# Kernel optimization log

Hardware: AMD Instinct MI355X
Metric: run time of the kernel (lower is better)

Reference implementation:

```python
import jax, jax.numpy as jnp
import numpy as np

B, I, O, DEG = 16384, 1024, 1024, 8

def setup_inputs() -> dict:
    key = jax.random.key(0)
    kx, kc = jax.random.split(key)
    x = jax.random.normal(kx, (B, I), dtype=jnp.float32)
    std = 1.0 / (I * (DEG + 1))
    cheby_coeffs = jax.random.normal(kc, (I, O, DEG + 1), dtype=jnp.float32) * std
    return {"x": x, "cheby_coeffs": cheby_coeffs}


def reference(x, cheby_coeffs):
    # Chebyshev basis: T_d(tanh(x)) = cos(d * acos(tanh(x)))
    deg = cheby_coeffs.shape[-1]
    arange = jnp.arange(deg, dtype=x.dtype)  # (D+1,)
    theta = jnp.arccos(jnp.tanh(x))          # (B, I)
    basis = jnp.cos(theta[:, :, None] * arange)  # (B, I, D+1)
    y = jnp.einsum('bid,iod->bo', basis, cheby_coeffs)
    return y
```

## Files before the change

kernel.cpp:

```cpp
#include <hip/hip_runtime.h>
#include <hip/hip_bf16.h>


#define WSCALE 4096.0f
#define INV_WSCALE (1.0f/4096.0f)

typedef _Float16 f16;
typedef __fp16   hf2  __attribute__((ext_vector_type(2)));
typedef _Float16 f16x8 __attribute__((ext_vector_type(8)));
typedef float    f32x4 __attribute__((ext_vector_type(4)));
typedef float    f32x16 __attribute__((ext_vector_type(16)));

union F16x8u { hf2 h2[4]; f16x8 v8; };

__global__ __launch_bounds__(256) void wt_transform(const float* __restrict__ cc,
                                                    f16* __restrict__ wt) {
  int t    = blockIdx.x * 256 + threadIdx.x;
  int j4   = t & 127;
  int grp  = t >> 7;
  int ncol = grp & 7;
  int rest = grp >> 3;
  int ic   = rest & 31;
  int d    = rest >> 5;
  int u    = j4 >> 5;
  int h    = (j4 >> 4) & 1;
  int r    = j4 & 15;
  int rk   = (r >> 1) & 3;
  size_t base = (size_t)(d * 32 + ic) * 32768 + (size_t)ncol * 4096 + (size_t)j4 * 32;
#pragma unroll
  for (int v = 0; v < 4; ++v) {
    int tt = v ^ rk;
    int q  = tt & 1, kl = tt >> 1;
    int o  = ncol * 128 + u * 32 + q * 16 + r;
    int ib = ic * 32 + h * 16 + kl * 8;
    f16x8 val;
#pragma unroll
    for (int e = 0; e < 8; ++e)
      val[e] = (f16)(cc[((size_t)(ib + e) * 1024 + o) * 9 + d] * WSCALE);
    *(f16x8*)(wt + base + v * 8) = val;
  }
}

__global__ __launch_bounds__(256) void t2_transform(const float* __restrict__ x,
                                                    f16* __restrict__ t2) {
  size_t gid = (size_t)blockIdx.x * 256 + threadIdx.x;
  const float* p = x + gid * 8;
  f32x4 a = *(const f32x4*)p;
  f32x4 b = *(const f32x4*)(p + 4);
  float tf[8];
#pragma unroll
  for (int e = 0; e < 8; ++e) {
    float xx = (e < 4) ? a[e] : b[e - 4];
    tf[e] = 1.f - 2.f * __builtin_amdgcn_rcpf(__expf(2.f * xx) + 1.f);
  }
  F16x8u u;
#pragma unroll
  for (int q = 0; q < 4; ++q)
    u.h2[q] = __builtin_amdgcn_cvt_pkrtz(tf[2 * q], tf[2 * q + 1]);
  f16x8 v = u.v8 + u.v8;
  *(f16x8*)(t2 + gid * 8) = v;
}

__global__ __launch_bounds__(256, 3) void cheby_gemm(const f16* __restrict__ t2g,
                                                     const f16* __restrict__ wt,
                                                     float* __restrict__ out) {
  __shared__ f16 bbuf[5][4096];

  const int tid  = threadIdx.x;
  const int wid  = tid >> 6;
  const int lane = tid & 63;
  const int lr   = lane & 31;
  const int lh   = lane >> 5;
  const int wm   = wid >> 1;
  const int wn   = wid & 1;
  const int mrow = blockIdx.x >> 3;
  const int ncol = blockIdx.x & 7;
  const int m0   = mrow * 128 + wm * 64;
  const int n0   = ncol * 128 + wn * 64;
  const int rbase = wn * 2048 + ((lane & 15) * 4 + ((lane >> 4) ^ ((lane >> 1) & 3))) * 8;

  auto stage = [&](int cn, int dn, int slot) {
    const f16* src = wt + (size_t)(dn * 32 + cn) * 32768 + (size_t)ncol * 4096;
    __builtin_amdgcn_global_load_lds(
        (const __attribute__((address_space(1))) unsigned*)(src + tid * 8),
        (__attribute__((address_space(3))) unsigned*)(&bbuf[slot][wid * 512]),
        16, 0, 0);
    __builtin_amdgcn_global_load_lds(
        (const __attribute__((address_space(1))) unsigned*)(src + 2048 + tid * 8),
        (__attribute__((address_space(3))) unsigned*)(&bbuf[slot][wid * 512 + 2048]),
        16, 0, 0);
  };

  f32x16 acc[2][2];
#pragma unroll
  for (int a = 0; a < 2; ++a)
#pragma unroll
    for (int b = 0; b < 2; ++b)
#pragma unroll
      for (int j = 0; j < 16; ++j) acc[a][b][j] = 0.f;

  const f16x8 ones  = {(f16)1,(f16)1,(f16)1,(f16)1,(f16)1,(f16)1,(f16)1,(f16)1};
  const f16x8 half8 = {(f16)0.5f,(f16)0.5f,(f16)0.5f,(f16)0.5f,
                       (f16)0.5f,(f16)0.5f,(f16)0.5f,(f16)0.5f};
  f16x8 t2v[2][2], t2n[2][2];

  auto loadx = [&](int cn) {
#pragma unroll
    for (int mb = 0; mb < 2; ++mb)
#pragma unroll
      for (int h = 0; h < 2; ++h)
        t2n[mb][h] = *(const f16x8*)(t2g + (size_t)(m0 + mb * 32 + lr) * 1024
                                         + cn * 32 + h * 16 + lh * 8);
  };

#define REC(NEW, S1, S2)                                                       \
  _Pragma("unroll") for (int mb = 0; mb < 2; ++mb)                             \
    _Pragma("unroll") for (int h = 0; h < 2; ++h)                              \
      NEW[mb][h] = __builtin_elementwise_fma(t2v[mb][h], S1[mb][h], -S2[mb][h]);

#define LOADB(BD, SLOT)                                                        \
  {                                                                            \
    const f16* bb = &bbuf[0][0] + (SLOT) * 4096 + rbase;                       \
    BD[0][0] = *(const f16x8*)&bb[0];    BD[0][1] = *(const f16x8*)&bb[512];   \
    BD[1][0] = *(const f16x8*)&bb[1024]; BD[1][1] = *(const f16x8*)&bb[1536];  \
  }

#define MFMA8(AF, BD)                                                          \
  {                                                                            \
    _Pragma("unroll") for (int nb = 0; nb < 2; ++nb)                           \
      _Pragma("unroll") for (int mb = 0; mb < 2; ++mb) {                       \
        acc[mb][nb] = __builtin_amdgcn_mfma_f32_32x32x16_f16(AF[mb][0], BD[nb][0], \
                                                             acc[mb][nb], 0, 0, 0); \
        acc[mb][nb] = __builtin_amdgcn_mfma_f32_32x32x16_f16(AF[mb][1], BD[nb][1], \
                                                             acc[mb][nb], 0, 0, 0); \
      }                                                                        \
  }

#define VMB(N)                                                                 \
  asm volatile("s_waitcnt vmcnt(" #N ")" ::: "memory");                        \
  __builtin_amdgcn_s_barrier();

  loadx(0);
  int p0 = 0, p1 = 1, p2 = 2, p3 = 3, p4 = 4;
  stage(0, 0, p0); stage(0, 1, p1); stage(0, 2, p2); stage(0, 3, p3);

  f16x8 onesA[2][2];
#pragma unroll
  for (int mb = 0; mb < 2; ++mb)
#pragma unroll
    for (int h = 0; h < 2; ++h) onesA[mb][h] = ones;

  f16x8 bfA[2][2], bfB[2][2];
  f16x8 A1[2][2], A2[2][2], A3[2][2], A4[2][2], A5[2][2], A6[2][2], A7[2][2], A8[2][2];

  for (int c = 0; c < 31; ++c) {
    VMB(4)
    LOADB(bfA, p0)
#pragma unroll
    for (int mb = 0; mb < 2; ++mb)
#pragma unroll
      for (int h = 0; h < 2; ++h) {
        t2v[mb][h] = t2n[mb][h];
        A1[mb][h]  = t2v[mb][h] * half8;
      }
    stage(c, 4, p4);
    loadx(c + 1);
    LOADB(bfB, p1)
    MFMA8(onesA, bfA)

    VMB(8) stage(c, 5, p0); LOADB(bfA, p2) REC(A2, A1, onesA) MFMA8(A1, bfB)
    VMB(8) stage(c, 6, p1); LOADB(bfB, p3) REC(A3, A2, A1)    MFMA8(A2, bfA)
    VMB(8) stage(c, 7, p2); LOADB(bfA, p4) REC(A4, A3, A2)    MFMA8(A3, bfB)
    VMB(4) stage(c, 8, p3); LOADB(bfB, p0) REC(A5, A4, A3)    MFMA8(A4, bfA)
    VMB(4) stage(c + 1, 0, p4); LOADB(bfA, p1) REC(A6, A5, A4) MFMA8(A5, bfB)
    VMB(4) stage(c + 1, 1, p0); LOADB(bfB, p2) REC(A7, A6, A5) MFMA8(A6, bfA)
    VMB(4) stage(c + 1, 2, p1); LOADB(bfA, p3) REC(A8, A7, A6) MFMA8(A7, bfB)
    stage(c + 1, 3, p2);
    MFMA8(A8, bfA)

    int tmp = p4; p4 = p3; p3 = p2; p2 = p1; p1 = p0; p0 = tmp;
  }

  {
    VMB(4)
    LOADB(bfA, p0)
#pragma unroll
    for (int mb = 0; mb < 2; ++mb)
#pragma unroll
      for (int h = 0; h < 2; ++h) {
        t2v[mb][h] = t2n[mb][h];
        A1[mb][h]  = t2v[mb][h] * half8;
      }
    stage(31, 4, p4);
    LOADB(bfB, p1)
    MFMA8(onesA, bfA)

    VMB(4) stage(31, 5, p0); LOADB(bfA, p2) REC(A2, A1, onesA) MFMA8(A1, bfB)
    VMB(4) stage(31, 6, p1); LOADB(bfB, p3) REC(A3, A2, A1)    MFMA8(A2, bfA)
    VMB(4) stage(31, 7, p2); LOADB(bfA, p4) REC(A4, A3, A2)    MFMA8(A3, bfB)
    VMB(4) stage(31, 8, p3); LOADB(bfB, p0) REC(A5, A4, A3)    MFMA8(A4, bfA)
    VMB(4) LOADB(bfA, p1) REC(A6, A5, A4) MFMA8(A5, bfB)
    VMB(2) LOADB(bfB, p2) REC(A7, A6, A5) MFMA8(A6, bfA)
    VMB(0) LOADB(bfA, p3) REC(A8, A7, A6) MFMA8(A7, bfB)
    MFMA8(A8, bfA)
  }
#undef REC
#undef LOADB
#undef MFMA8
#undef VMB

#pragma unroll
  for (int mb = 0; mb < 2; ++mb)
#pragma unroll
    for (int nb = 0; nb < 2; ++nb)
#pragma unroll
      for (int j = 0; j < 16; ++j) {
        int row = m0 + mb * 32 + 4 * lh + (j & 3) + 8 * (j >> 2);
        int col = n0 + nb * 32 + lr;
        out[(size_t)row * 1024 + col] = acc[mb][nb][j] * INV_WSCALE;
      }
}

__global__ __launch_bounds__(512, 2) void cheby_gemm_fb(const float* __restrict__ x,
                                                        const f16* __restrict__ wt,
                                                        float* __restrict__ out) {
  __shared__ f16 bbuf[18][4096];
  const int tid  = threadIdx.x;
  const int wid  = tid >> 6;
  const int lane = tid & 63;
  const int lr   = lane & 31;
  const int lh   = lane >> 5;
  const int wm   = wid >> 1;
  const int wn   = wid & 1;
  const int mrow = blockIdx.x >> 3;
  const int ncol = blockIdx.x & 7;
  const int m0   = mrow * 256 + wm * 64;
  const int n0   = ncol * 128 + wn * 64;
  const int rbase = wn * 2048 + ((lane & 15) * 4 + ((lane >> 4) ^ ((lane >> 1) & 3))) * 8;

  auto stage = [&](int cn, int dn, int buf) {
    const f16* src = wt + (size_t)(dn * 32 + cn) * 32768 + (size_t)ncol * 4096;
    __builtin_amdgcn_global_load_lds(
        (const __attribute__((address_space(1))) unsigned*)(src + tid * 8),
        (__attribute__((address_space(3))) unsigned*)(&bbuf[buf][wid * 512]),
        16, 0, 0);
  };
  auto stage9 = [&](int cn, int b0) {
#pragma unroll
    for (int d = 0; d < 9; ++d) stage(cn, d, b0 + d);
  };

  f32x16 acc[2][2];
#pragma unroll
  for (int a = 0; a < 2; ++a)
#pragma unroll
    for (int b = 0; b < 2; ++b)
#pragma unroll
      for (int j = 0; j < 16; ++j) acc[a][b][j] = 0.f;

  const f16x8 ones  = {(f16)1,(f16)1,(f16)1,(f16)1,(f16)1,(f16)1,(f16)1,(f16)1};
  const f16x8 half8 = {(f16)0.5f,(f16)0.5f,(f16)0.5f,(f16)0.5f,
                       (f16)0.5f,(f16)0.5f,(f16)0.5f,(f16)0.5f};
  f16x8 t2v[2][2], t2n[2][2];
  f32x4 xf[2][2][2];

  auto loadx = [&](int cn) {
#pragma unroll
    for (int mb = 0; mb < 2; ++mb)
#pragma unroll
      for (int h = 0; h < 2; ++h) {
        const float* p = x + (size_t)(m0 + mb * 32 + lr) * 1024 + cn * 32 + h * 16 + lh * 8;
        xf[mb][h][0] = *(const f32x4*)p;
        xf[mb][h][1] = *(const f32x4*)(p + 4);
      }
  };
  auto dotanh = [&]() {
#pragma unroll
    for (int mb = 0; mb < 2; ++mb)
#pragma unroll
      for (int h = 0; h < 2; ++h) {
        float tf[8];
#pragma unroll
        for (int e = 0; e < 8; ++e) {
          float xx = (e < 4) ? xf[mb][h][0][e] : xf[mb][h][1][e - 4];
          tf[e] = 1.f - 2.f * __builtin_amdgcn_rcpf(__expf(2.f * xx) + 1.f);
        }
        F16x8u u;
#pragma unroll
        for (int q = 0; q < 4; ++q)
          u.h2[q] = __builtin_amdgcn_cvt_pkrtz(tf[2 * q], tf[2 * q + 1]);
        t2n[mb][h] = u.v8 + u.v8;
      }
  };

#define REC(NEW, S1, S2)                                                       \
  _Pragma("unroll") for (int mb = 0; mb < 2; ++mb)                             \
    _Pragma("unroll") for (int h = 0; h < 2; ++h)                              \
      NEW[mb][h] = __builtin_elementwise_fma(t2v[mb][h], S1[mb][h], -S2[mb][h]);
#define CLUSTER(AF, DIDX)                                                      \
  {                                                                            \
    const f16* bb = &bbuf[0][0] + sbase + (DIDX) * 4096 + rbase;               \
    f16x8 bf[2][2];                                                            \
    _Pragma("unroll") for (int nb = 0; nb < 2; ++nb)                           \
      _Pragma("unroll") for (int h = 0; h < 2; ++h)                            \
        bf[nb][h] = *(const f16x8*)&bb[nb * 1024 + h * 512];                   \
    _Pragma("unroll") for (int nb = 0; nb < 2; ++nb)                           \
      _Pragma("unroll") for (int mb = 0; mb < 2; ++mb) {                       \
        acc[mb][nb] = __builtin_amdgcn_mfma_f32_32x32x16_f16(AF[mb][0], bf[nb][0], \
                                                             acc[mb][nb], 0, 0, 0); \
        acc[mb][nb] = __builtin_amdgcn_mfma_f32_32x32x16_f16(AF[mb][1], bf[nb][1], \
                                                             acc[mb][nb], 0, 0, 0); \
      }                                                                        \
  }

  stage9(0, 0);
  loadx(0);
  dotanh();

  f16x8 onesA[2][2];
#pragma unroll
  for (int mb = 0; mb < 2; ++mb)
#pragma unroll
    for (int h = 0; h < 2; ++h) onesA[mb][h] = ones;

  for (int c = 0; c < 32; ++c) {
    const bool lastc = (c == 31);
    const int  sbase = (c & 1) * 36864;
    const int  nbase = (1 - (c & 1)) * 9;

    asm volatile("s_waitcnt vmcnt(8)" ::: "memory");
    __builtin_amdgcn_s_barrier();

    f16x8 A1[2][2], A2[2][2], A3[2][2], A4[2][2], A5[2][2], A6[2][2], A7[2][2], A8[2][2];
#pragma unroll
    for (int mb = 0; mb < 2; ++mb)
#pragma unroll
      for (int h = 0; h < 2; ++h) {
        t2v[mb][h] = t2n[mb][h];
        A1[mb][h]  = t2v[mb][h] * half8;
      }
    if (!lastc) { stage9(c + 1, nbase); loadx(c + 1); }

    CLUSTER(onesA, 0)
    CLUSTER(A1, 1)
    REC(A2, A1, onesA)  CLUSTER(A2, 2)
    REC(A3, A2, A1)     CLUSTER(A3, 3)
    REC(A4, A3, A2)     CLUSTER(A4, 4)
    REC(A5, A4, A3)     CLUSTER(A5, 5)
    REC(A6, A5, A4)     CLUSTER(A6, 6)
    REC(A7, A6, A5)     CLUSTER(A7, 7)
    REC(A8, A7, A6)     CLUSTER(A8, 8)
    if (!lastc) dotanh();
  }
#undef REC
#undef CLUSTER

#pragma unroll
  for (int mb = 0; mb < 2; ++mb)
#pragma unroll
    for (int nb = 0; nb < 2; ++nb)
#pragma unroll
      for (int j = 0; j < 16; ++j) {
        int row = m0 + mb * 32 + 4 * lh + (j & 3) + 8 * (j >> 2);
        int col = n0 + nb * 32 + lr;
        out[(size_t)row * 1024 + col] = acc[mb][nb][j] * INV_WSCALE;
      }
}

extern "C" void kernel_launch(void* const* d_in, const int* in_sizes, int n_in,
                              void* d_out, int out_size, void* d_ws, size_t ws_size,
                              hipStream_t stream) {
  const float* x  = (const float*)d_in[0];
  const float* cc = (const float*)d_in[1];
  f16*   wt  = (f16*)d_ws;
  f16*   t2  = (f16*)((char*)d_ws + 18874368);
  float* out = (float*)d_out;

  hipLaunchKernelGGL(wt_transform, dim3(1152), dim3(256), 0, stream, cc, wt);
  if (ws_size >= 52428800) {
    hipLaunchKernelGGL(t2_transform, dim3(8192), dim3(256), 0, stream, x, t2);
    hipLaunchKernelGGL(cheby_gemm, dim3(1024), dim3(256), 0, stream, t2, wt, out);
  } else {
    hipLaunchKernelGGL(cheby_gemm_fb, dim3(512), dim3(512), 0, stream, x, wt, out);
  }
}
```

Before: 331.7 us.

## Coalesce weight transform via LDS and deepen GEMM LDS pipeline to six slots

```diff
diff --git a/kernel.cpp b/kernel.cpp
--- a/kernel.cpp
+++ b/kernel.cpp
@@ -7,37 +7,70 @@
 
 typedef _Float16 f16;
 typedef __fp16   hf2  __attribute__((ext_vector_type(2)));
+typedef _Float16 f16x2v __attribute__((ext_vector_type(2)));
 typedef _Float16 f16x8 __attribute__((ext_vector_type(8)));
 typedef float    f32x4 __attribute__((ext_vector_type(4)));
+typedef float    f32x4u __attribute__((ext_vector_type(4), aligned(4)));
+typedef float    f32x2u __attribute__((ext_vector_type(2), aligned(4)));
 typedef float    f32x16 __attribute__((ext_vector_type(16)));
 
 union F16x8u { hf2 h2[4]; f16x8 v8; };
 
 __global__ __launch_bounds__(256) void wt_transform(const float* __restrict__ cc,
                                                     f16* __restrict__ wt) {
-  int t    = blockIdx.x * 256 + threadIdx.x;
-  int j4   = t & 127;
-  int grp  = t >> 7;
-  int ncol = grp & 7;
-  int rest = grp >> 3;
-  int ic   = rest & 31;
-  int d    = rest >> 5;
-  int u    = j4 >> 5;
-  int h    = (j4 >> 4) & 1;
-  int r    = j4 & 15;
-  int rk   = (r >> 1) & 3;
-  size_t base = (size_t)(d * 32 + ic) * 32768 + (size_t)ncol * 4096 + (size_t)j4 * 32;
-#pragma unroll
-  for (int v = 0; v < 4; ++v) {
-    int tt = v ^ rk;
-    int q  = tt & 1, kl = tt >> 1;
-    int o  = ncol * 128 + u * 32 + q * 16 + r;
-    int ib = ic * 32 + h * 16 + kl * 8;
-    f16x8 val;
-#pragma unroll
-    for (int e = 0; e < 8; ++e)
-      val[e] = (f16)(cc[((size_t)(ib + e) * 1024 + o) * 9 + d] * WSCALE);
-    *(f16x8*)(wt + base + v * 8) = val;
+  __shared__ f16 s16[9216];
+  const int bid  = blockIdx.x;
+  const int u    = bid & 3;
+  const int ncol = (bid >> 2) & 7;
+  const int ic   = bid >> 5;
+  const int t    = threadIdx.x;
+  const int i2   = t >> 4;
+  const int o2   = t & 15;
+  const int i0   = i2 * 2, o0 = o2 * 2;
+  const int h    = i0 >> 4;
+  const int kl   = (i0 >> 3) & 1;
+  const int e    = i0 & 7;
+
+  float va[2][18];
+#pragma unroll
+  for (int ii = 0; ii < 2; ++ii) {
+    const float* g = cc + ((size_t)(ic * 32 + i0 + ii) * 1024
+                           + (ncol * 128 + u * 32 + o0)) * 9;
+    f32x4u a = *(const f32x4u*)(g);
+    f32x4u b = *(const f32x4u*)(g + 4);
+    f32x4u c4 = *(const f32x4u*)(g + 8);
+    f32x4u d4 = *(const f32x4u*)(g + 12);
+    f32x2u e2 = *(const f32x2u*)(g + 16);
+#pragma unroll
+    for (int j = 0; j < 4; ++j) { va[ii][j] = a[j]; va[ii][4 + j] = b[j];
+                                  va[ii][8 + j] = c4[j]; va[ii][12 + j] = d4[j]; }
+    va[ii][16] = e2[0]; va[ii][17] = e2[1];
+  }
+
+#pragma unroll
+  for (int oo = 0; oo < 2; ++oo) {
+    const int ol = o0 + oo;
+    const int r  = ol & 15, q = ol >> 4;
+    const int rk = (r >> 1) & 3;
+    const int vsl = (kl * 2 + q) ^ rk;
+    const int jj = h * 16 + r;
+#pragma unroll
+    for (int d = 0; d < 9; ++d) {
+      f16x2v pv = { (f16)(va[0][oo * 9 + d] * WSCALE),
+                    (f16)(va[1][oo * 9 + d] * WSCALE) };
+      *(f16x2v*)(&s16[(d * 128 + jj * 4 + vsl) * 8 + e]) = pv;
+    }
+  }
+  __syncthreads();
+
+#pragma unroll
+  for (int w = 0; w < 5; ++w) {
+    int cidx = t + 256 * w;
+    if (cidx < 1152) {
+      f16x8 val = *(const f16x8*)(&s16[cidx * 8]);
+      int d = cidx >> 7, rem = cidx & 127;
+      *(f16x8*)(wt + (size_t)((d * 32 + ic) * 8 + ncol) * 4096 + u * 1024 + rem * 8) = val;
+    }
   }
 }
 
@@ -64,7 +97,7 @@
 __global__ __launch_bounds__(256, 3) void cheby_gemm(const f16* __restrict__ t2g,
                                                      const f16* __restrict__ wt,
                                                      float* __restrict__ out) {
-  __shared__ f16 bbuf[5][4096];
+  __shared__ f16 bbuf[6][4096];
 
   const int tid  = threadIdx.x;
   const int wid  = tid >> 6;
@@ -118,14 +151,14 @@
     _Pragma("unroll") for (int h = 0; h < 2; ++h)                              \
       NEW[mb][h] = __builtin_elementwise_fma(t2v[mb][h], S1[mb][h], -S2[mb][h]);
 
-#define LOADB(BD, SLOT)                                                        \
+#define LB(BD, SLOT)                                                           \
   {                                                                            \
     const f16* bb = &bbuf[0][0] + (SLOT) * 4096 + rbase;                       \
     BD[0][0] = *(const f16x8*)&bb[0];    BD[0][1] = *(const f16x8*)&bb[512];   \
     BD[1][0] = *(const f16x8*)&bb[1024]; BD[1][1] = *(const f16x8*)&bb[1536];  \
   }
 
-#define MFMA8(AF, BD)                                                          \
+#define M8(AF, BD)                                                             \
   {                                                                            \
     _Pragma("unroll") for (int nb = 0; nb < 2; ++nb)                           \
       _Pragma("unroll") for (int mb = 0; mb < 2; ++mb) {                       \
@@ -136,77 +169,69 @@
       }                                                                        \
   }
 
+#define ADOPT                                                                  \
+  _Pragma("unroll") for (int mb = 0; mb < 2; ++mb)                             \
+    _Pragma("unroll") for (int h = 0; h < 2; ++h) {                            \
+      t2v[mb][h] = t2n[mb][h];                                                 \
+      A1[mb][h]  = t2v[mb][h] * half8;                                         \
+    }
+
 #define VMB(N)                                                                 \
   asm volatile("s_waitcnt vmcnt(" #N ")" ::: "memory");                        \
   __builtin_amdgcn_s_barrier();
 
+  f16x8 onesA[2][2];
+#pragma unroll
+  for (int mb = 0; mb < 2; ++mb)
+#pragma unroll
+    for (int h = 0; h < 2; ++h) onesA[mb][h] = ones;
+
+  f16x8 bf0[2][2], bf1[2][2], bf2[2][2];
+  f16x8 A1[2][2], A2[2][2], A3[2][2], A4[2][2], A5[2][2], A6[2][2], A7[2][2], A8[2][2];
+  int q0 = 0, q1 = 1, q2 = 2, q3 = 3, q4 = 4, q5 = 5;
+
   loadx(0);
-  int p0 = 0, p1 = 1, p2 = 2, p3 = 3, p4 = 4;
-  stage(0, 0, p0); stage(0, 1, p1); stage(0, 2, p2); stage(0, 3, p3);
-
-  f16x8 onesA[2][2];
-#pragma unroll
-  for (int mb = 0; mb < 2; ++mb)
-#pragma unroll
-    for (int h = 0; h < 2; ++h) onesA[mb][h] = ones;
-
-  f16x8 bfA[2][2], bfB[2][2];
-  f16x8 A1[2][2], A2[2][2], A3[2][2], A4[2][2], A5[2][2], A6[2][2], A7[2][2], A8[2][2];
+  stage(0, 0, 0); stage(0, 1, 1); stage(0, 2, 2); stage(0, 3, 3); stage(0, 4, 4);
+  VMB(6)
+  LB(bf0, 0) LB(bf1, 1)
+
+  VMB(4)
+  LB(bf2, q2)
+  ADOPT
+  stage(0, 5, q5);
+  M8(onesA, bf0)
 
   for (int c = 0; c < 31; ++c) {
+    VMB(4) stage(c, 6, q0); loadx(c + 1); LB(bf0, q3) REC(A2, A1, onesA) M8(A1, bf1)
+    VMB(8) stage(c, 7, q1);     LB(bf1, q4) REC(A3, A2, A1) M8(A2, bf2)
+    VMB(8) stage(c, 8, q2);     LB(bf2, q5) REC(A4, A3, A2) M8(A3, bf0)
+    VMB(8) stage(c + 1, 0, q3); LB(bf0, q0) REC(A5, A4, A3) M8(A4, bf1)
+    VMB(4) stage(c + 1, 1, q4); LB(bf1, q1) REC(A6, A5, A4) M8(A5, bf2)
+    VMB(4) stage(c + 1, 2, q5); LB(bf2, q2) REC(A7, A6, A5) M8(A6, bf0)
+    VMB(4) stage(c + 1, 3, q0); LB(bf0, q3) REC(A8, A7, A6) M8(A7, bf1)
+    VMB(4) stage(c + 1, 4, q1); LB(bf1, q4)                 M8(A8, bf2)
+    { int r0 = q0, r1 = q1, r2 = q2;
+      q0 = q3; q1 = q4; q2 = q5; q3 = r0; q4 = r1; q5 = r2; }
     VMB(4)
-    LOADB(bfA, p0)
-#pragma unroll
-    for (int mb = 0; mb < 2; ++mb)
-#pragma unroll
-      for (int h = 0; h < 2; ++h) {
-        t2v[mb][h] = t2n[mb][h];
-        A1[mb][h]  = t2v[mb][h] * half8;
-      }
-    stage(c, 4, p4);
-    loadx(c + 1);
-    LOADB(bfB, p1)
-    MFMA8(onesA, bfA)
-
-    VMB(8) stage(c, 5, p0); LOADB(bfA, p2) REC(A2, A1, onesA) MFMA8(A1, bfB)
-    VMB(8) stage(c, 6, p1); LOADB(bfB, p3) REC(A3, A2, A1)    MFMA8(A2, bfA)
-    VMB(8) stage(c, 7, p2); LOADB(bfA, p4) REC(A4, A3, A2)    MFMA8(A3, bfB)
-    VMB(4) stage(c, 8, p3); LOADB(bfB, p0) REC(A5, A4, A3)    MFMA8(A4, bfA)
-    VMB(4) stage(c + 1, 0, p4); LOADB(bfA, p1) REC(A6, A5, A4) MFMA8(A5, bfB)
-    VMB(4) stage(c + 1, 1, p0); LOADB(bfB, p2) REC(A7, A6, A5) MFMA8(A6, bfA)
-    VMB(4) stage(c + 1, 2, p1); LOADB(bfA, p3) REC(A8, A7, A6) MFMA8(A7, bfB)
-    stage(c + 1, 3, p2);
-    MFMA8(A8, bfA)
-
-    int tmp = p4; p4 = p3; p3 = p2; p2 = p1; p1 = p0; p0 = tmp;
-  }
-
-  {
-    VMB(4)
-    LOADB(bfA, p0)
-#pragma unroll
-    for (int mb = 0; mb < 2; ++mb)
-#pragma unroll
-      for (int h = 0; h < 2; ++h) {
-        t2v[mb][h] = t2n[mb][h];
-        A1[mb][h]  = t2v[mb][h] * half8;
-      }
-    stage(31, 4, p4);
-    LOADB(bfB, p1)
-    MFMA8(onesA, bfA)
-
-    VMB(4) stage(31, 5, p0); LOADB(bfA, p2) REC(A2, A1, onesA) MFMA8(A1, bfB)
-    VMB(4) stage(31, 6, p1); LOADB(bfB, p3) REC(A3, A2, A1)    MFMA8(A2, bfA)
-    VMB(4) stage(31, 7, p2); LOADB(bfA, p4) REC(A4, A3, A2)    MFMA8(A3, bfB)
-    VMB(4) stage(31, 8, p3); LOADB(bfB, p0) REC(A5, A4, A3)    MFMA8(A4, bfA)
-    VMB(4) LOADB(bfA, p1) REC(A6, A5, A4) MFMA8(A5, bfB)
-    VMB(2) LOADB(bfB, p2) REC(A7, A6, A5) MFMA8(A6, bfA)
-    VMB(0) LOADB(bfA, p3) REC(A8, A7, A6) MFMA8(A7, bfB)
-    MFMA8(A8, bfA)
-  }
+    LB(bf2, q2)
+    ADOPT
+    stage(c + 1, 5, q5);
+    M8(onesA, bf0)
+  }
+
+  VMB(4) stage(31, 6, q0); LB(bf0, q3) REC(A2, A1, onesA) M8(A1, bf1)
+  VMB(4) stage(31, 7, q1); LB(bf1, q4) REC(A3, A2, A1)    M8(A2, bf2)
+  VMB(4) stage(31, 8, q2); LB(bf2, q5) REC(A4, A3, A2)    M8(A3, bf0)
+  VMB(4) LB(bf0, q0) REC(A5, A4, A3) M8(A4, bf1)
+  VMB(2) LB(bf1, q1) REC(A6, A5, A4) M8(A5, bf2)
+  VMB(0) LB(bf2, q2) REC(A7, A6, A5) M8(A6, bf0)
+  REC(A8, A7, A6) M8(A7, bf1)
+  M8(A8, bf2)
+
 #undef REC
-#undef LOADB
-#undef MFMA8
+#undef LB
+#undef M8
+#undef ADOPT
 #undef VMB
 
 #pragma unroll
@@ -376,7 +401,7 @@
   f16*   t2  = (f16*)((char*)d_ws + 18874368);
   float* out = (float*)d_out;
 
-  hipLaunchKernelGGL(wt_transform, dim3(1152), dim3(256), 0, stream, cc, wt);
+  hipLaunchKernelGGL(wt_transform, dim3(1024), dim3(256), 0, stream, cc, wt);
   if (ws_size >= 52428800) {
     hipLaunchKernelGGL(t2_transform, dim3(8192), dim3(256), 0, stream, x, t2);
     hipLaunchKernelGGL(cheby_gemm, dim3(1024), dim3(256), 0, stream, t2, wt, out);
```

Measured after the change: 301.0 us. 9.3% less time.
